# Kernel optimization log

Measured on AMD Instinct MI355X. Metric: run time of the kernel, lower is better.

Reference implementation:

```python
import jax, jax.numpy as jnp
import numpy as np

DEPTH = 12
N_FEATURES = 512
BATCH = 16384
N_NODES = 2 ** DEPTH - 1   # 4095 internal nodes, concatenated level-by-level
N_LEAVES = 2 ** DEPTH      # 4096


def setup_inputs() -> dict:
    key = jax.random.key(0)
    k_x, k_w, k_b, k_s, k_l = jax.random.split(key, 5)
    x_input = jax.random.normal(k_x, (BATCH, N_FEATURES), dtype=jnp.float32)
    # Per-level Linear(n_features, 2**d) weights concatenated on the output dim:
    # level d occupies rows [2**d - 1, 2**(d+1) - 1).
    bound = 1.0 / np.sqrt(N_FEATURES)  # torch Linear default init scale
    W_all = jax.random.uniform(k_w, (N_NODES, N_FEATURES), dtype=jnp.float32,
                               minval=-bound, maxval=bound)
    b_all = jax.random.uniform(k_b, (N_NODES,), dtype=jnp.float32,
                               minval=-bound, maxval=bound)
    # original uses max(randn, 1) -> positive steepness >= 1
    s_all = jax.random.uniform(k_s, (N_NODES,), dtype=jnp.float32,
                               minval=1.0, maxval=2.0)
    leaves = jax.random.normal(k_l, (N_LEAVES,), dtype=jnp.float32)
    return {"x_input": x_input, "W_all": W_all, "b_all": b_all,
            "s_all": s_all, "leaves": leaves}


def reference(x_input, W_all, b_all, s_all, leaves):
    B = x_input.shape[0]
    # One fused GEMM for all depth levels: [B, 2**depth - 1]
    logits = x_input @ W_all.T + b_all
    p_all = jax.nn.sigmoid(logits * s_all)
    # Recursive path-probability product down the binary tree.
    # out[:, j] at level d is the prob of reaching child j (j = 2*node + side),
    # matching the original dict insertion order (node ascending, left then right).
    out = jnp.ones((B, 1), dtype=p_all.dtype)
    for d in range(DEPTH):
        start = 2 ** d - 1
        p = p_all[:, start:start + 2 ** d]          # [B, 2**d]
        # interleave left (parent*p) and right (parent*(1-p)) children
        out = jnp.stack([out * p, out * (1.0 - p)], axis=-1).reshape(B, 2 ** (d + 1))
    # weighted sum over leaves
    return (jax.nn.sigmoid(leaves) * out).sum(axis=1)   # [B]
```

## Files before the change

kernel.cpp:

```cpp
#include <hip/hip_runtime.h>
#include <hip/hip_bf16.h>

#define M_DIM   16384
#define K_DIM   512
#define NNODES  4095
#define NPERM   4096
#define NTOP    128
#define NWROWS  (NPERM + NTOP)
#define NBOT_BLOCKS (32 * 128)
#define NTOT_BLOCKS (NBOT_BLOCKS + 128)

typedef __bf16   bf16x8 __attribute__((ext_vector_type(8)));
typedef float    floatx4 __attribute__((ext_vector_type(4)));

__device__ __forceinline__ float sigmoidf_(float z) {
    return __builtin_amdgcn_rcpf(1.f + __expf(-z));
}

__device__ __forceinline__ void gld_lds16(const void* g, void* l) {
    __builtin_amdgcn_global_load_lds(
        (const __attribute__((address_space(1))) void*)g,
        (__attribute__((address_space(3))) void*)l, 16, 0, 0);
}

__global__ __launch_bounds__(256) void cvt_all(const float* __restrict__ X,
                                               const float* __restrict__ W,
                                               const float* __restrict__ bias,
                                               const float* __restrict__ scale,
                                               __hip_bfloat16* __restrict__ Xb,
                                               __hip_bfloat16* __restrict__ Wb,
                                               float* __restrict__ bp,
                                               float* __restrict__ sp) {
    const int bid = blockIdx.x;
    if (bid < 4096) {
        const int idx = (bid * 256 + threadIdx.x) * 8;
        float4 f0 = *reinterpret_cast<const float4*>(X + idx);
        float4 f1 = *reinterpret_cast<const float4*>(X + idx + 4);
        __hip_bfloat16 h[8];
        h[0] = __float2bfloat16(f0.x); h[1] = __float2bfloat16(f0.y);
        h[2] = __float2bfloat16(f0.z); h[3] = __float2bfloat16(f0.w);
        h[4] = __float2bfloat16(f1.x); h[5] = __float2bfloat16(f1.y);
        h[6] = __float2bfloat16(f1.z); h[7] = __float2bfloat16(f1.w);
        *reinterpret_cast<int4*>(Xb + idx) = *reinterpret_cast<int4*>(h);
        return;
    }
    const int idx = ((bid - 4096) * 256 + threadIdx.x) * 8;
    const int r = idx >> 9;
    const int k = idx & 511;
    int node;
    if (r < NPERM) {
        const int t = r >> 5, o = r & 31;
        int d, q;
        if (o < 16)       { d = 11; q = o; }
        else if (o < 24)  { d = 10; q = o - 16; }
        else if (o < 28)  { d = 9;  q = o - 24; }
        else if (o < 30)  { d = 8;  q = o - 28; }
        else if (o == 30) { d = 7;  q = 0; }
        else              { d = -1; q = 0; }
        node = (d < 0) ? -1 : ((1 << d) - 1 + (t << (d - 7)) + q);
    } else {
        const int c = r - NPERM;
        node = (c < 127) ? c : -1;
    }
    __hip_bfloat16 h[8];
    if (node >= 0) {
        const float* src = W + (size_t)node * 512 + k;
        float4 f0 = *reinterpret_cast<const float4*>(src);
        float4 f1 = *reinterpret_cast<const float4*>(src + 4);
        h[0] = __float2bfloat16(f0.x); h[1] = __float2bfloat16(f0.y);
        h[2] = __float2bfloat16(f0.z); h[3] = __float2bfloat16(f0.w);
        h[4] = __float2bfloat16(f1.x); h[5] = __float2bfloat16(f1.y);
        h[6] = __float2bfloat16(f1.z); h[7] = __float2bfloat16(f1.w);
    } else {
        #pragma unroll
        for (int i = 0; i < 8; ++i) h[i] = __float2bfloat16(0.f);
    }
    *reinterpret_cast<int4*>(Wb + idx) = *reinterpret_cast<int4*>(h);
    if (k == 0) {
        bp[r] = (node >= 0) ? bias[node]  : 0.f;
        sp[r] = (node >= 0) ? scale[node] : 1.f;
    }
}

#define PT_STRIDE 135
#define BUFB 32768
__global__ __launch_bounds__(256) void gemm_fold(
    const __hip_bfloat16* __restrict__ A,
    const __hip_bfloat16* __restrict__ B,
    const float* __restrict__ bp,
    const float* __restrict__ sp,
    const float* __restrict__ leaves,
    float* __restrict__ partial,
    _Float16* __restrict__ ptop)
{
    __shared__ char smem[66560] __attribute__((aligned(16)));
    _Float16* pt  = (_Float16*)smem;
    float*    slf = (float*)(smem + 66048);

    const int tid  = threadIdx.x;
    const int lane = tid & 63;
    const int wv   = tid >> 6;
    const int bid  = blockIdx.x;
    int tile_m, tile_n;
    if (bid < NBOT_BLOCKS) { tile_m = bid >> 5; tile_n = bid & 31; }
    else                   { tile_m = bid - NBOT_BLOCKS; tile_n = 32; }
    const int m0 = tile_m * 128;
    const int n0 = tile_n * 128;

    if (tile_n < 32 && tid < 128) slf[tid] = sigmoidf_(leaves[n0 + tid]);

    const int wm = (wv >> 1) * 64;
    const int wn = (wv & 1) * 64;
    const int lrow = lane >> 3;
    const int swzb = ((lane & 7) ^ lrow) * 16;
    const int quad = lane >> 4;
    const int l15  = lane & 15;
    const int xr   = l15 & 7;

    const char* gAp[4];
    const char* gBp[4];
    char* sA[4];
    char* sB[4];
    #pragma unroll
    for (int i = 0; i < 4; ++i) {
        const int rbase = i * 32 + wv * 8;
        gAp[i] = (const char*)(A + (size_t)(m0 + rbase + lrow) * K_DIM) + swzb;
        gBp[i] = (const char*)(B + (size_t)(n0 + rbase + lrow) * K_DIM) + swzb;
        sA[i] = smem + rbase * 128;
        sB[i] = smem + 16384 + rbase * 128;
    }

    floatx4 acc[4][4];
    #pragma unroll
    for (int i = 0; i < 4; ++i)
        #pragma unroll
        for (int j = 0; j < 4; ++j)
            acc[i][j] = (floatx4){0.f, 0.f, 0.f, 0.f};

    #pragma unroll
    for (int i = 0; i < 4; ++i) {
        gld_lds16(gAp[i], sA[i]);
        gld_lds16(gBp[i], sB[i]);
        gAp[i] += 128; gBp[i] += 128;
    }

    #pragma unroll 1
    for (int k0 = 0; k0 < 8; ++k0) {
        __syncthreads();
        if (k0 < 7) {
            const int boff = ((k0 + 1) & 1) * BUFB;
            #pragma unroll
            for (int i = 0; i < 4; ++i) {
                gld_lds16(gAp[i], sA[i] + boff);
                gld_lds16(gBp[i], sB[i] + boff);
                gAp[i] += 128; gBp[i] += 128;
            }
        }
        const __hip_bfloat16* cA =
            (const __hip_bfloat16*)(smem + (k0 & 1) * BUFB);
        const __hip_bfloat16* cB = cA + 8192;
        #pragma unroll
        for (int kk = 0; kk < 64; kk += 32) {
            const int cb = ((kk >> 3) + quad) ^ xr;
            bf16x8 af[4], bfr[4];
            #pragma unroll
            for (int i = 0; i < 4; ++i)
                af[i] = *reinterpret_cast<const bf16x8*>(
                    &cA[(wm + i * 16 + l15) * 64 + cb * 8]);
            #pragma unroll
            for (int j = 0; j < 4; ++j)
                bfr[j] = *reinterpret_cast<const bf16x8*>(
                    &cB[(wn + j * 16 + l15) * 64 + cb * 8]);
            #pragma unroll
            for (int i = 0; i < 4; ++i)
                #pragma unroll
                for (int j = 0; j < 4; ++j)
                    acc[i][j] = __builtin_amdgcn_mfma_f32_16x16x32_bf16(
                        af[i], bfr[j], acc[i][j], 0, 0, 0);
        }
    }
    __syncthreads();

    float bn[4], sn[4];
    #pragma unroll
    for (int j = 0; j < 4; ++j) {
        const int n = n0 + wn + j * 16 + l15;
        bn[j] = bp[n];
        sn[j] = sp[n];
    }

    if (tile_n == 32) {
        #pragma unroll
        for (int i = 0; i < 4; ++i) {
            #pragma unroll
            for (int r = 0; r < 4; ++r) {
                const int m = m0 + wm + i * 16 + quad * 4 + r;
                #pragma unroll
                for (int j = 0; j < 4; ++j) {
                    const int col = wn + j * 16 + l15;
                    ptop[(size_t)m * 128 + col] =
                        (_Float16)sigmoidf_((acc[i][j][r] + bn[j]) * sn[j]);
                }
            }
        }
        return;
    }

    #pragma unroll
    for (int i = 0; i < 4; ++i) {
        #pragma unroll
        for (int r = 0; r < 4; ++r) {
            const int row = wm + i * 16 + quad * 4 + r;
            #pragma unroll
            for (int j = 0; j < 4; ++j) {
                const int col = wn + j * 16 + l15;
                pt[row * PT_STRIDE + col] =
                    (_Float16)sigmoidf_((acc[i][j][r] + bn[j]) * sn[j]);
            }
        }
    }
    __syncthreads();

    #pragma unroll
    for (int z = 0; z < 2; ++z) {
        const int task = tid + z * 256;
        const int row  = task >> 2;
        const int t    = task & 3;
        const _Float16* pp = pt + row * PT_STRIDE + t * 32;
        const float*    sl = slf + t * 32;
        float v[16];
        #pragma unroll
        for (int q = 0; q < 16; ++q) {
            const float p = (float)pp[q];
            v[q] = p * sl[2 * q] + (1.f - p) * sl[2 * q + 1];
        }
        #pragma unroll
        for (int q = 0; q < 8; ++q) {
            const float p = (float)pp[16 + q];
            v[q] = p * v[2 * q] + (1.f - p) * v[2 * q + 1];
        }
        #pragma unroll
        for (int q = 0; q < 4; ++q) {
            const float p = (float)pp[24 + q];
            v[q] = p * v[2 * q] + (1.f - p) * v[2 * q + 1];
        }
        #pragma unroll
        for (int q = 0; q < 2; ++q) {
            const float p = (float)pp[28 + q];
            v[q] = p * v[2 * q] + (1.f - p) * v[2 * q + 1];
        }
        const float p7 = (float)pp[30];
        partial[(size_t)(m0 + row) * 128 + tile_n * 4 + t] =
            p7 * v[0] + (1.f - p7) * v[1];
    }
}

__global__ __launch_bounds__(256) void final_fold(
    const float* __restrict__ partial,
    const _Float16* __restrict__ ptop,
    float* __restrict__ out)
{
    __shared__ float    pL[64 * 129];
    __shared__ _Float16 pq[64 * 134];

    const int tid = threadIdx.x;
    const int m0  = blockIdx.x * 64;

    #pragma unroll
    for (int it = 0; it < 32; ++it) {
        const int idx = tid + it * 256;
        const int row = idx >> 7;
        const int c   = idx & 127;
        pL[row * 129 + c] = partial[(size_t)(m0 + row) * 128 + c];
        pq[row * 134 + c] = ptop[(size_t)(m0 + row) * 128 + c];
    }
    __syncthreads();

    if (tid < 64) {
        float* v = pL + tid * 129;
        const _Float16* pr = pq + tid * 134;
        #pragma unroll
        for (int d = 6; d >= 1; --d) {
            const int base = (1 << d) - 1;
            const int cnt  = 1 << d;
            for (int q = 0; q < cnt; ++q) {
                const float p = (float)pr[base + q];
                v[q] = p * v[2 * q] + (1.f - p) * v[2 * q + 1];
            }
        }
        const float p0 = (float)pr[0];
        out[m0 + tid] = p0 * v[0] + (1.f - p0) * v[1];
    }
}

__global__ __launch_bounds__(256) void tnn_fallback(
    const float* __restrict__ X, const float* __restrict__ W,
    const float* __restrict__ bias, const float* __restrict__ scale,
    const float* __restrict__ leaves, float* __restrict__ out)
{
    __shared__ float xr[512];
    __shared__ float sl[4096];
    __shared__ float pp[4096];
    __shared__ float v0[2048];
    __shared__ float v1[1024];
    const int tid  = threadIdx.x;
    const int lane = tid & 63;
    const int wv   = tid >> 6;
    const int b    = blockIdx.x;
    for (int i = tid; i < 512;  i += 256) xr[i] = X[(size_t)b * 512 + i];
    for (int i = tid; i < 4096; i += 256) sl[i] = sigmoidf_(leaves[i]);
    __syncthreads();
    for (int n = wv; n < NNODES; n += 4) {
        float sum = 0.f;
        const float* wr = W + (size_t)n * 512;
        for (int k = lane; k < 512; k += 64) sum += xr[k] * wr[k];
        #pragma unroll
        for (int off = 32; off; off >>= 1) sum += __shfl_xor(sum, off);
        if (lane == 0) pp[n] = sigmoidf_((sum + bias[n]) * scale[n]);
    }
    __syncthreads();
    for (int j = tid; j < 2048; j += 256) {
        const float p = pp[2047 + j];
        v0[j] = p * sl[2 * j] + (1.f - p) * sl[2 * j + 1];
    }
    __syncthreads();
    float* src = v0;
    float* dst = v1;
    for (int d = 10; d >= 0; --d) {
        const int width = 1 << d;
        const int start = width - 1;
        for (int j = tid; j < width; j += 256) {
            const float p = pp[start + j];
            dst[j] = p * src[2 * j] + (1.f - p) * src[2 * j + 1];
        }
        __syncthreads();
        float* t = src; src = dst; dst = t;
    }
    if (tid == 0) out[b] = src[0];
}

extern "C" void kernel_launch(void* const* d_in, const int* in_sizes, int n_in,
                              void* d_out, int out_size, void* d_ws, size_t ws_size,
                              hipStream_t stream) {
    const float* X      = (const float*)d_in[0];
    const float* W      = (const float*)d_in[1];
    const float* bias   = (const float*)d_in[2];
    const float* scale  = (const float*)d_in[3];
    const float* leaves = (const float*)d_in[4];
    float* out = (float*)d_out;

    const size_t offX  = 0;
    const size_t offW  = (size_t)M_DIM * K_DIM * 2;
    const size_t offB  = offW + (size_t)NWROWS * K_DIM * 2;
    const size_t offS  = offB + (size_t)NWROWS * 4;
    const size_t offP  = offS + (size_t)NWROWS * 4;
    const size_t offT  = offP + (size_t)M_DIM * 128 * 4;
    const size_t need  = offT + (size_t)M_DIM * 128 * 2;

    if (ws_size >= need) {
        __hip_bfloat16* Xb = (__hip_bfloat16*)((char*)d_ws + offX);
        __hip_bfloat16* Wb = (__hip_bfloat16*)((char*)d_ws + offW);
        float* bp = (float*)((char*)d_ws + offB);
        float* sp = (float*)((char*)d_ws + offS);
        float* partial = (float*)((char*)d_ws + offP);
        _Float16* ptop = (_Float16*)((char*)d_ws + offT);
        cvt_all<<<4096 + 1056, 256, 0, stream>>>(X, W, bias, scale, Xb, Wb, bp, sp);
        gemm_fold<<<NTOT_BLOCKS, 256, 0, stream>>>(
            Xb, Wb, bp, sp, leaves, partial, ptop);
        final_fold<<<M_DIM / 64, 256, 0, stream>>>(partial, ptop, out);
    } else {
        tnn_fallback<<<M_DIM, 256, 0, stream>>>(X, W, bias, scale, leaves, out);
    }
}
```

Measured before the change: 190.4 us.

## Fuse convert, GEMM and fold stages into one cooperative persistent kernel

Merges the three launches (bf16 conversion, GEMM with tree fold, final fold) into one cooperative kernel. A persistent grid of up to 512 blocks loops over work units, with grid-wide syncs between stages. This removes two kernel launch gaps and the tail effects between stages. The cost is grid-sync overhead, fewer resident blocks for the GEMM stage than the original 4224-block launch (less latency hiding), and a host-side occupancy query on every call. The final fold now uses 32-row units, so its fallback launch has 512 blocks.

```diff
diff --git a/kernel.cpp b/kernel.cpp
--- a/kernel.cpp
+++ b/kernel.cpp
@@ -1,5 +1,8 @@
 #include <hip/hip_runtime.h>
 #include <hip/hip_bf16.h>
+#include <hip/hip_cooperative_groups.h>
+
+namespace cg = cooperative_groups;
 
 #define M_DIM   16384
 #define K_DIM   512
@@ -9,6 +12,8 @@
 #define NWROWS  (NPERM + NTOP)
 #define NBOT_BLOCKS (32 * 128)
 #define NTOT_BLOCKS (NBOT_BLOCKS + 128)
+#define NCVT_UNITS  (4096 + 1056)
+#define NFOLD_UNITS 512
 
 typedef __bf16   bf16x8 __attribute__((ext_vector_type(8)));
 typedef float    floatx4 __attribute__((ext_vector_type(4)));
@@ -23,15 +28,16 @@
         (__attribute__((address_space(3))) void*)l, 16, 0, 0);
 }
 
-__global__ __launch_bounds__(256) void cvt_all(const float* __restrict__ X,
-                                               const float* __restrict__ W,
-                                               const float* __restrict__ bias,
-                                               const float* __restrict__ scale,
-                                               __hip_bfloat16* __restrict__ Xb,
-                                               __hip_bfloat16* __restrict__ Wb,
-                                               float* __restrict__ bp,
-                                               float* __restrict__ sp) {
-    const int bid = blockIdx.x;
+
+__device__ __forceinline__ void cvt_unit(int bid,
+                                         const float* __restrict__ X,
+                                         const float* __restrict__ W,
+                                         const float* __restrict__ bias,
+                                         const float* __restrict__ scale,
+                                         __hip_bfloat16* __restrict__ Xb,
+                                         __hip_bfloat16* __restrict__ Wb,
+                                         float* __restrict__ bp,
+                                         float* __restrict__ sp) {
     if (bid < 4096) {
         const int idx = (bid * 256 + threadIdx.x) * 8;
         float4 f0 = *reinterpret_cast<const float4*>(X + idx);
@@ -84,7 +90,8 @@
 
 #define PT_STRIDE 135
 #define BUFB 32768
-__global__ __launch_bounds__(256) void gemm_fold(
+__device__ __forceinline__ void gemm_tile(
+    int bid, char* smem,
     const __hip_bfloat16* __restrict__ A,
     const __hip_bfloat16* __restrict__ B,
     const float* __restrict__ bp,
@@ -93,14 +100,12 @@
     float* __restrict__ partial,
     _Float16* __restrict__ ptop)
 {
-    __shared__ char smem[66560] __attribute__((aligned(16)));
     _Float16* pt  = (_Float16*)smem;
     float*    slf = (float*)(smem + 66048);
 
     const int tid  = threadIdx.x;
     const int lane = tid & 63;
     const int wv   = tid >> 6;
-    const int bid  = blockIdx.x;
     int tile_m, tile_n;
     if (bid < NBOT_BLOCKS) { tile_m = bid >> 5; tile_n = bid & 31; }
     else                   { tile_m = bid - NBOT_BLOCKS; tile_n = 32; }
@@ -255,30 +260,27 @@
     }
 }
 
-__global__ __launch_bounds__(256) void final_fold(
-    const float* __restrict__ partial,
-    const _Float16* __restrict__ ptop,
-    float* __restrict__ out)
-{
-    __shared__ float    pL[64 * 129];
-    __shared__ _Float16 pq[64 * 134];
-
+__device__ __forceinline__ void fold_unit32(int u, char* smem,
+                                            const float* __restrict__ partial,
+                                            const _Float16* __restrict__ ptop,
+                                            float* __restrict__ out)
+{
+    float*    fL = (float*)smem;
+    _Float16* fq = (_Float16*)(smem + 16512);
     const int tid = threadIdx.x;
-    const int m0  = blockIdx.x * 64;
-
-    #pragma unroll
-    for (int it = 0; it < 32; ++it) {
+    const int r0  = u * 32;
+    #pragma unroll
+    for (int it = 0; it < 16; ++it) {
         const int idx = tid + it * 256;
         const int row = idx >> 7;
         const int c   = idx & 127;
-        pL[row * 129 + c] = partial[(size_t)(m0 + row) * 128 + c];
-        pq[row * 134 + c] = ptop[(size_t)(m0 + row) * 128 + c];
-    }
-    __syncthreads();
-
-    if (tid < 64) {
-        float* v = pL + tid * 129;
-        const _Float16* pr = pq + tid * 134;
+        fL[row * 129 + c] = partial[(size_t)(r0 + row) * 128 + c];
+        fq[row * 134 + c] = ptop[(size_t)(r0 + row) * 128 + c];
+    }
+    __syncthreads();
+    if (tid < 32) {
+        float* v = fL + tid * 129;
+        const _Float16* pr = fq + tid * 134;
         #pragma unroll
         for (int d = 6; d >= 1; --d) {
             const int base = (1 << d) - 1;
@@ -289,8 +291,66 @@
             }
         }
         const float p0 = (float)pr[0];
-        out[m0 + tid] = p0 * v[0] + (1.f - p0) * v[1];
-    }
+        out[r0 + tid] = p0 * v[0] + (1.f - p0) * v[1];
+    }
+}
+
+__global__ __launch_bounds__(256) void tnn_coop(
+    const float* __restrict__ X, const float* __restrict__ W,
+    const float* __restrict__ bias, const float* __restrict__ scale,
+    const float* __restrict__ leaves,
+    __hip_bfloat16* __restrict__ Xb, __hip_bfloat16* __restrict__ Wb,
+    float* __restrict__ bp, float* __restrict__ sp,
+    float* __restrict__ partial, _Float16* __restrict__ ptop,
+    float* __restrict__ out)
+{
+    __shared__ char smem[66560] __attribute__((aligned(16)));
+
+    for (int bu = blockIdx.x; bu < NCVT_UNITS; bu += gridDim.x)
+        cvt_unit(bu, X, W, bias, scale, Xb, Wb, bp, sp);
+
+    cg::this_grid().sync();
+
+    for (int tb = blockIdx.x; tb < NTOT_BLOCKS; tb += gridDim.x) {
+        gemm_tile(tb, smem, Xb, Wb, bp, sp, leaves, partial, ptop);
+        __syncthreads();
+    }
+
+    cg::this_grid().sync();
+
+    for (int u = blockIdx.x; u < NFOLD_UNITS; u += gridDim.x) {
+        fold_unit32(u, smem, partial, ptop, out);
+        __syncthreads();
+    }
+}
+
+__global__ __launch_bounds__(256) void cvt_all(const float* __restrict__ X,
+                                               const float* __restrict__ W,
+                                               const float* __restrict__ bias,
+                                               const float* __restrict__ scale,
+                                               __hip_bfloat16* __restrict__ Xb,
+                                               __hip_bfloat16* __restrict__ Wb,
+                                               float* __restrict__ bp,
+                                               float* __restrict__ sp) {
+    cvt_unit(blockIdx.x, X, W, bias, scale, Xb, Wb, bp, sp);
+}
+
+__global__ __launch_bounds__(256) void gemm_fold(
+    const __hip_bfloat16* __restrict__ A, const __hip_bfloat16* __restrict__ B,
+    const float* __restrict__ bp, const float* __restrict__ sp,
+    const float* __restrict__ leaves, float* __restrict__ partial,
+    _Float16* __restrict__ ptop)
+{
+    __shared__ char smem[66560] __attribute__((aligned(16)));
+    gemm_tile(blockIdx.x, smem, A, B, bp, sp, leaves, partial, ptop);
+}
+
+__global__ __launch_bounds__(256) void final_fold(
+    const float* __restrict__ partial, const _Float16* __restrict__ ptop,
+    float* __restrict__ out)
+{
+    __shared__ char smem[25088] __attribute__((aligned(16)));
+    fold_unit32(blockIdx.x, smem, partial, ptop, out);
 }
 
 __global__ __launch_bounds__(256) void tnn_fallback(
@@ -357,18 +417,37 @@
     const size_t offT  = offP + (size_t)M_DIM * 128 * 4;
     const size_t need  = offT + (size_t)M_DIM * 128 * 2;
 
-    if (ws_size >= need) {
-        __hip_bfloat16* Xb = (__hip_bfloat16*)((char*)d_ws + offX);
-        __hip_bfloat16* Wb = (__hip_bfloat16*)((char*)d_ws + offW);
-        float* bp = (float*)((char*)d_ws + offB);
-        float* sp = (float*)((char*)d_ws + offS);
-        float* partial = (float*)((char*)d_ws + offP);
-        _Float16* ptop = (_Float16*)((char*)d_ws + offT);
-        cvt_all<<<4096 + 1056, 256, 0, stream>>>(X, W, bias, scale, Xb, Wb, bp, sp);
+    if (ws_size < need) {
+        tnn_fallback<<<M_DIM, 256, 0, stream>>>(X, W, bias, scale, leaves, out);
+        return;
+    }
+
+    __hip_bfloat16* Xb = (__hip_bfloat16*)((char*)d_ws + offX);
+    __hip_bfloat16* Wb = (__hip_bfloat16*)((char*)d_ws + offW);
+    float* bp = (float*)((char*)d_ws + offB);
+    float* sp = (float*)((char*)d_ws + offS);
+    float* partial = (float*)((char*)d_ws + offP);
+    _Float16* ptop = (_Float16*)((char*)d_ws + offT);
+
+    int maxb = 0;
+    hipError_t oq = hipOccupancyMaxActiveBlocksPerMultiprocessor(
+        &maxb, reinterpret_cast<const void*>(tnn_coop), 256, 0);
+    bool coop_ok = false;
+    if (oq == hipSuccess && maxb >= 1) {
+        int grid = 256 * maxb;
+        if (grid > 512) grid = 512;
+        void* args[] = { (void*)&X, (void*)&W, (void*)&bias, (void*)&scale,
+                         (void*)&leaves, (void*)&Xb, (void*)&Wb, (void*)&bp,
+                         (void*)&sp, (void*)&partial, (void*)&ptop, (void*)&out };
+        hipError_t lr = hipLaunchCooperativeKernel(
+            reinterpret_cast<const void*>(tnn_coop),
+            dim3(grid), dim3(256), args, 0, stream);
+        coop_ok = (lr == hipSuccess);
+    }
+    if (!coop_ok) {
+        cvt_all<<<NCVT_UNITS, 256, 0, stream>>>(X, W, bias, scale, Xb, Wb, bp, sp);
         gemm_fold<<<NTOT_BLOCKS, 256, 0, stream>>>(
             Xb, Wb, bp, sp, leaves, partial, ptop);
-        final_fold<<<M_DIM / 64, 256, 0, stream>>>(partial, ptop, out);
-    } else {
-        tnn_fallback<<<M_DIM, 256, 0, stream>>>(X, W, bias, scale, leaves, out);
-    }
-}
+        final_fold<<<NFOLD_UNITS, 256, 0, stream>>>(partial, ptop, out);
+    }
+}
```

New measurement: 317.0 us. 66.4% more time.
